# Optimization experiments

Hardware: AMD Instinct MI355X
Metric: run time of the kernel (lower is better)

Reference implementation:

```python
import jax, jax.numpy as jnp
import numpy as np

K = 16       # hidden size k
STATE = 8    # state_size

def _pre(x, W1, b1, W2, b2):
    # PreProcess: two Linear+ReLU layers
    return jax.nn.relu(jax.nn.relu(x @ W1 + b1) @ W2 + b2)

def _dblock(x, W1, b1, W2, b2, Wmu, bmu, Wls, bls):
    # DBlock (TD-VAE style): gated hidden then mu / logsigma heads
    t = jnp.tanh(x @ W1 + b1) * jax.nn.sigmoid(x @ W2 + b2)
    return t @ Wmu + bmu, t @ Wls + bls

def setup_inputs() -> dict:
    key = jax.random.key(0)
    ks = iter(jax.random.split(key, 40))
    L, B, IN, OBS = 1000, 1024, 8, 4
    def w(shape):
        return (jax.random.normal(next(ks), shape, jnp.float32) / np.sqrt(shape[0])).astype(jnp.float32)
    z = lambda n: jnp.zeros((n,), jnp.float32)
    return {
        "external_input_seq": jax.random.normal(next(ks), (L, B, IN), jnp.float32),
        "observations_seq":   jax.random.normal(next(ks), (L, B, OBS), jnp.float32),
        "eps":                jax.random.normal(next(ks), (L, B, STATE), jnp.float32),
        # process_u / process_x / process_z (PreProcess)
        "pu_W1": w((IN, K)),  "pu_b1": z(K), "pu_W2": w((K, K)), "pu_b2": z(K),
        "px_W1": w((OBS, K)), "px_b1": z(K), "px_W2": w((K, K)), "px_b2": z(K),
        "pz_W1": w((STATE, K)), "pz_b1": z(K), "pz_W2": w((K, K)), "pz_b2": z(K),
        # posterior_gauss: DBlock(3k, 3k, state_size)
        "post_W1": w((3*K, 3*K)), "post_b1": z(3*K),
        "post_W2": w((3*K, 3*K)), "post_b2": z(3*K),
        "post_Wmu": w((3*K, STATE)), "post_bmu": z(STATE),
        "post_Wls": w((3*K, STATE)), "post_bls": z(STATE),
        # rnn: tanh RNN cell, input 3k -> hidden k, 1 layer
        "rnn_Wih": w((3*K, K)), "rnn_bih": z(K),
        "rnn_Whh": w((K, K)),   "rnn_bhh": z(K),
    }

def reference(external_input_seq, observations_seq, eps,
              pu_W1, pu_b1, pu_W2, pu_b2,
              px_W1, px_b1, px_W2, px_b2,
              pz_W1, pz_b1, pz_W2, pz_b2,
              post_W1, post_b1, post_W2, post_b2,
              post_Wmu, post_bmu, post_Wls, post_bls,
              rnn_Wih, rnn_bih, rnn_Whh, rnn_bhh):
    # forward_posterior with memory_state=None
    L, B, _ = external_input_seq.shape
    u_e = _pre(external_input_seq, pu_W1, pu_b1, pu_W2, pu_b2)  # [L,B,K] (precomputed, as in torch)
    x_e = _pre(observations_seq, px_W1, px_b1, px_W2, px_b2)    # [L,B,K]
    h0 = jnp.zeros((B, K), external_input_seq.dtype)

    def step(h, inputs):
        xe_t, ue_t, eps_t = inputs  # [B,K],[B,K],[B,STATE]
        mu, ls = _dblock(jnp.concatenate([xe_t, ue_t, h], -1),
                         post_W1, post_b1, post_W2, post_b2,
                         post_Wmu, post_bmu, post_Wls, post_bls)
        # reparameterized sample from N(mu, diag(exp(ls))) -> std = exp(0.5*ls)
        z_t = mu + jnp.exp(0.5 * ls) * eps_t
        z_e = _pre(z_t, pz_W1, pz_b1, pz_W2, pz_b2)
        rnn_in = jnp.concatenate([xe_t, ue_t, z_e], -1)  # [B,3K]
        h_new = jnp.tanh(rnn_in @ rnn_Wih + rnn_bih + h @ rnn_Whh + rnn_bhh)
        return h_new, (mu, ls)

    h_final, (state_mu, state_logsigma) = jax.lax.scan(step, h0, (x_e, u_e, eps))
    # returns (state_mu, state_logsigma, memory_state hn); rnn_hidden == hn[None] for 1 layer
    return state_mu, state_logsigma, h_final
```

## Files before the change

### kernel.cpp

```cpp
#include <hip/hip_runtime.h>

#define L_STEPS 1000
#define BATCH   1024

__device__ __forceinline__ float frcp(float x)  { return __builtin_amdgcn_rcpf(x); }
__device__ __forceinline__ float fsig(float x)  { return frcp(1.0f + __expf(-x)); }
__device__ __forceinline__ float ftanh(float x) { return 1.0f - 2.0f * frcp(__expf(2.0f * x) + 1.0f); }

#define FMA4(vv, W, base, A) do { \
    A = fmaf((vv).x, W[(base)+0], A); \
    A = fmaf((vv).y, W[(base)+1], A); \
    A = fmaf((vv).z, W[(base)+2], A); \
    A = fmaf((vv).w, W[(base)+3], A); } while (0)

__global__ __launch_bounds__(64, 1) void vrnn_scan(
    const float* __restrict__ ext, const float* __restrict__ obs, const float* __restrict__ eps,
    const float* __restrict__ puW1, const float* __restrict__ pub1,
    const float* __restrict__ puW2, const float* __restrict__ pub2,
    const float* __restrict__ pxW1, const float* __restrict__ pxb1,
    const float* __restrict__ pxW2, const float* __restrict__ pxb2,
    const float* __restrict__ pzW1, const float* __restrict__ pzb1,
    const float* __restrict__ pzW2, const float* __restrict__ pzb2,
    const float* __restrict__ poW1, const float* __restrict__ pob1,
    const float* __restrict__ poW2, const float* __restrict__ pob2,
    const float* __restrict__ Wmu, const float* __restrict__ bmu,
    const float* __restrict__ Wls, const float* __restrict__ bls,
    const float* __restrict__ Wih, const float* __restrict__ bih,
    const float* __restrict__ Whh, const float* __restrict__ bhh,
    float* __restrict__ out)
{
    const int l   = threadIdx.x;
    const int r   = blockIdx.x;
    const int idx = l >> 2;
    const int p   = l & 3;

    __shared__ __align__(16) float rawbuf[16];
    __shared__ __align__(16) float epsbuf[8];
    __shared__ __align__(16) float h1buf[32];
    __shared__ __align__(16) float in64[64];
    __shared__ __align__(16) float s2buf[48];
    __shared__ __align__(16) float t48[48];
    __shared__ __align__(16) float zbuf[8];
    __shared__ __align__(16) float ze1buf[16];
    __shared__ float bheadb[16];
    __shared__ float brnnb[16];

    if (l < 16) {
        rawbuf[l]    = 0.0f;
        in64[48 + l] = 0.0f;
        bheadb[l]    = (l < 8) ? bmu[l] : bls[l - 8];
        brnnb[l]     = bih[l] + bhh[l];
    }

    float wA[48]; float biasA;
    {
        const float* baseA;
        if (l < 48) { baseA = poW1 + l;        biasA = pob1[l]; }
        else        { baseA = poW2 + (l - 48); biasA = pob2[l - 48]; }
        #pragma unroll
        for (int k = 0; k < 48; ++k) wA[k] = baseA[k * 48];
    }
    float wB[48]; float biasB;
    {
        const int c = 16 + (l & 31);
        const float* baseB = poW2 + c;
        biasB = pob2[c];
        #pragma unroll
        for (int k = 0; k < 48; ++k) wB[k] = baseB[k * 48];
    }
    float whead[12];
    {
        const float* baseH = (idx < 8) ? (Wmu + idx) : (Wls + (idx - 8));
        #pragma unroll
        for (int i = 0; i < 12; ++i) whead[i] = baseH[(12 * p + i) * 8];
    }
    float wrnn[16];
    {
        #pragma unroll
        for (int i = 0; i < 16; ++i) {
            const int c = 16 * p + i;
            const float a = Wih[min(c, 47) * 16 + idx];
            const float b = Whh[max(c - 48, 0) * 16 + idx];
            wrnn[i] = (c < 48) ? a : b;
        }
    }
    const int j16 = l & 15;
    float wpre1[8], wpre2[16], bpre1, bpre2;
    {
        const bool isx = (l < 16);
        #pragma unroll
        for (int k = 0; k < 8; ++k) {
            const float xv = pxW1[min(k, 3) * 16 + j16];
            const float uv = puW1[k * 16 + j16];
            float v = isx ? xv : uv;
            if (isx && k >= 4) v = 0.0f;
            wpre1[k] = v;
        }
        #pragma unroll
        for (int k = 0; k < 16; ++k) {
            const float xv = pxW2[k * 16 + j16];
            const float uv = puW2[k * 16 + j16];
            wpre2[k] = isx ? xv : uv;
        }
        bpre1 = isx ? pxb1[j16] : pub1[j16];
        bpre2 = isx ? pxb2[j16] : pub2[j16];
    }
    float wpz1[8], wpz2[16], bpz1, bpz2;
    {
        #pragma unroll
        for (int k = 0; k < 8; ++k)  wpz1[k] = pzW1[k * 16 + j16];
        #pragma unroll
        for (int k = 0; k < 16; ++k) wpz2[k] = pzW2[k * 16 + j16];
        bpz1 = pzb1[j16];
        bpz2 = pzb2[j16];
    }

    const float* pin; long pstride;
    if (l < 4)                  { pin = obs + (size_t)r * 4 + l;        pstride = 4 * BATCH; }
    else if (l >= 8 && l < 16)  { pin = ext + (size_t)r * 8 + (l - 8);  pstride = 8 * BATCH; }
    else if (l >= 16 && l < 24) { pin = eps + (size_t)r * 8 + (l - 16); pstride = 8 * BATCH; }
    else                        { pin = obs;                            pstride = 0; }

    float vin = *pin;
    pin += pstride;

    float* pout = out + ((idx < 8) ? ((size_t)r * 8 + idx)
                                   : ((size_t)L_STEPS * BATCH * 8 + (size_t)r * 8 + (idx - 8)));

    __syncthreads();

    float hn = 0.0f;

    for (int t = 0; t < L_STEPS; ++t) {
        if (l < 4 || (l >= 8 && l < 16)) rawbuf[l] = vin;
        if (l >= 16 && l < 24)           epsbuf[l - 16] = vin;
        vin = *pin;
        pin += (t < L_STEPS - 2) ? pstride : 0;

        {
            const float4* rb = (const float4*)(rawbuf + ((l & 16) ? 8 : 0));
            float4 v0 = rb[0], v1 = rb[1];
            float a1 = bpre1;
            FMA4(v0, wpre1, 0, a1);
            FMA4(v1, wpre1, 4, a1);
            a1 = fmaxf(a1, 0.0f);
            if (l < 32) h1buf[l] = a1;
            const float4* hb = (const float4*)(h1buf + ((l & 16) ? 16 : 0));
            float a2 = bpre2;
            #pragma unroll
            for (int q = 0; q < 4; ++q) { float4 v = hb[q]; FMA4(v, wpre2, 4 * q, a2); }
            a2 = fmaxf(a2, 0.0f);
            if (l < 32) in64[l] = a2;
        }

        float sA = biasA, sB = biasB;
        {
            const float4* c4 = (const float4*)in64;
            #pragma unroll
            for (int q = 0; q < 8; ++q) {
                float4 v = c4[q];
                FMA4(v, wA, 4 * q, sA);
                FMA4(v, wB, 4 * q, sB);
            }
            const float4* h4 = (const float4*)(in64 + 48);
            #pragma unroll
            for (int q = 0; q < 4; ++q) {
                float4 v = h4[q];
                FMA4(v, wA, 32 + 4 * q, sA);
                FMA4(v, wB, 32 + 4 * q, sB);
            }
        }
        if (l >= 48) s2buf[l - 48] = sA;
        if (l < 32)  s2buf[16 + l] = sB;
        if (l < 48)  t48[l] = ftanh(sA) * fsig(s2buf[l]);

        float acc = 0.0f;
        {
            const float4* tb = (const float4*)(t48 + 12 * p);
            float4 a0 = tb[0], a1v = tb[1], a2v = tb[2];
            FMA4(a0,  whead, 0, acc);
            FMA4(a1v, whead, 4, acc);
            FMA4(a2v, whead, 8, acc);
        }
        acc += __shfl_xor(acc, 1);
        acc += __shfl_xor(acc, 2);
        acc += bheadb[idx];
        if (p == 0) *pout = acc;
        pout += (size_t)8 * BATCH;

        {
            float lsv = __shfl(acc, l | 32);
            if (l < 32) {
                float z = fmaf(__expf(0.5f * lsv), epsbuf[idx], acc);
                if (p == 0) zbuf[idx] = z;
            }
        }

        {
            const float4* zb = (const float4*)zbuf;
            float4 z0 = zb[0], z1 = zb[1];
            float a1 = bpz1;
            FMA4(z0, wpz1, 0, a1);
            FMA4(z1, wpz1, 4, a1);
            a1 = fmaxf(a1, 0.0f);
            if (l < 16) ze1buf[l] = a1;
            const float4* zeb = (const float4*)ze1buf;
            float a2 = bpz2;
            #pragma unroll
            for (int q = 0; q < 4; ++q) { float4 v = zeb[q]; FMA4(v, wpz2, 4 * q, a2); }
            a2 = fmaxf(a2, 0.0f);
            if (l < 16) in64[32 + l] = a2;
        }

        {
            const float4* ib = (const float4*)(in64 + 16 * p);
            float a = 0.0f;
            #pragma unroll
            for (int q = 0; q < 4; ++q) { float4 v = ib[q]; FMA4(v, wrnn, 4 * q, a); }
            a += __shfl_xor(a, 1);
            a += __shfl_xor(a, 2);
            a += brnnb[idx];
            hn = ftanh(a);
            if (p == 0) in64[48 + idx] = hn;
        }
    }

    if (p == 0) out[(size_t)L_STEPS * BATCH * 8 * 2 + (size_t)r * 16 + idx] = hn;
}

extern "C" void kernel_launch(void* const* d_in, const int* in_sizes, int n_in,
                              void* d_out, int out_size, void* d_ws, size_t ws_size,
                              hipStream_t stream) {
    const float* ext  = (const float*)d_in[0];
    const float* obs  = (const float*)d_in[1];
    const float* eps  = (const float*)d_in[2];
    const float* puW1 = (const float*)d_in[3];  const float* pub1 = (const float*)d_in[4];
    const float* puW2 = (const float*)d_in[5];  const float* pub2 = (const float*)d_in[6];
    const float* pxW1 = (const float*)d_in[7];  const float* pxb1 = (const float*)d_in[8];
    const float* pxW2 = (const float*)d_in[9];  const float* pxb2 = (const float*)d_in[10];
    const float* pzW1 = (const float*)d_in[11]; const float* pzb1 = (const float*)d_in[12];
    const float* pzW2 = (const float*)d_in[13]; const float* pzb2 = (const float*)d_in[14];
    const float* poW1 = (const float*)d_in[15]; const float* pob1 = (const float*)d_in[16];
    const float* poW2 = (const float*)d_in[17]; const float* pob2 = (const float*)d_in[18];
    const float* Wmu  = (const float*)d_in[19]; const float* bmu  = (const float*)d_in[20];
    const float* Wls  = (const float*)d_in[21]; const float* bls  = (const float*)d_in[22];
    const float* Wih  = (const float*)d_in[23]; const float* bih  = (const float*)d_in[24];
    const float* Whh  = (const float*)d_in[25]; const float* bhh  = (const float*)d_in[26];
    float* out = (float*)d_out;

    vrnn_scan<<<dim3(BATCH), dim3(64), 0, stream>>>(
        ext, obs, eps,
        puW1, pub1, puW2, pub2,
        pxW1, pxb1, pxW2, pxb2,
        pzW1, pzb1, pzW2, pzb2,
        poW1, pob1, poW2, pob2,
        Wmu, bmu, Wls, bls,
        Wih, bih, Whh, bhh,
        out);
}
```

Measured before the change: 1.350 ms.

## Precompute time-parallel projections in a separate kernel before the recurrent scan

Adds a fully parallel pre-pass kernel that computes the x/u preprocessing plus their contributions to the posterior gates and the RNN input projection for every timestep, and stores them in a 128-float-per-row workspace. A new scan kernel then only does the h-dependent work each step: it reads the precomputed partial sums with one-step-ahead prefetch and uses DPP quad reductions and shuffles across a 4-lane split. This takes the non-recurrent matmuls off the serial critical path. In exchange it writes and reads roughly half a gigabyte of workspace, and it falls back to the old kernel when the workspace is too small.

```diff
diff --git a/kernel.cpp b/kernel.cpp
--- a/kernel.cpp
+++ b/kernel.cpp
@@ -2,16 +2,242 @@
 
 #define L_STEPS 1000
 #define BATCH   1024
+#define REC     128
 
 __device__ __forceinline__ float frcp(float x)  { return __builtin_amdgcn_rcpf(x); }
 __device__ __forceinline__ float fsig(float x)  { return frcp(1.0f + __expf(-x)); }
 __device__ __forceinline__ float ftanh(float x) { return 1.0f - 2.0f * frcp(__expf(2.0f * x) + 1.0f); }
+
+__device__ __forceinline__ float qxor1(float x) {
+    return __int_as_float(__builtin_amdgcn_update_dpp(0, __float_as_int(x), 0xB1, 0xF, 0xF, true));
+}
+__device__ __forceinline__ float qxor2(float x) {
+    return __int_as_float(__builtin_amdgcn_update_dpp(0, __float_as_int(x), 0x4E, 0xF, 0xF, true));
+}
 
 #define FMA4(vv, W, base, A) do { \
     A = fmaf((vv).x, W[(base)+0], A); \
     A = fmaf((vv).y, W[(base)+1], A); \
     A = fmaf((vv).z, W[(base)+2], A); \
     A = fmaf((vv).w, W[(base)+3], A); } while (0)
+
+__global__ __launch_bounds__(128) void vrnn_pre(
+    const float* __restrict__ ext, const float* __restrict__ obs,
+    const float* __restrict__ puW1, const float* __restrict__ pub1,
+    const float* __restrict__ puW2, const float* __restrict__ pub2,
+    const float* __restrict__ pxW1, const float* __restrict__ pxb1,
+    const float* __restrict__ pxW2, const float* __restrict__ pxb2,
+    const float* __restrict__ poW1, const float* __restrict__ pob1,
+    const float* __restrict__ poW2, const float* __restrict__ pob2,
+    const float* __restrict__ Wih, const float* __restrict__ bih,
+    const float* __restrict__ bhh,
+    float* __restrict__ ws)
+{
+    const int j  = threadIdx.x;
+    const int rc = blockIdx.x * 128;
+    const int t  = blockIdx.y;
+
+    __shared__ float wsm[768];
+    __shared__ float xu[128][36];
+
+    for (int i = j; i < 64;  i += 128) wsm[0   + i] = pxW1[i];
+    for (int i = j; i < 256; i += 128) wsm[64  + i] = pxW2[i];
+    for (int i = j; i < 128; i += 128) wsm[320 + i] = puW1[i];
+    for (int i = j; i < 256; i += 128) wsm[448 + i] = puW2[i];
+    if (j < 16) {
+        wsm[704 + j] = pxb1[j]; wsm[720 + j] = pxb2[j];
+        wsm[736 + j] = pub1[j]; wsm[752 + j] = pub2[j];
+    }
+    __syncthreads();
+
+    {
+        const size_t row = (size_t)t * BATCH + rc + j;
+        const float* o = obs + row * 4;
+        const float* e = ext + row * 8;
+        float ob[4], ex[8];
+        #pragma unroll
+        for (int k = 0; k < 4; ++k) ob[k] = o[k];
+        #pragma unroll
+        for (int k = 0; k < 8; ++k) ex[k] = e[k];
+
+        float t1[16];
+        #pragma unroll
+        for (int c = 0; c < 16; ++c) {
+            float a = wsm[704 + c];
+            #pragma unroll
+            for (int k = 0; k < 4; ++k) a = fmaf(ob[k], wsm[0 + k * 16 + c], a);
+            t1[c] = fmaxf(a, 0.0f);
+        }
+        #pragma unroll
+        for (int c = 0; c < 16; ++c) {
+            float a = wsm[720 + c];
+            #pragma unroll
+            for (int k = 0; k < 16; ++k) a = fmaf(t1[k], wsm[64 + k * 16 + c], a);
+            xu[j][c] = fmaxf(a, 0.0f);
+        }
+        #pragma unroll
+        for (int c = 0; c < 16; ++c) {
+            float a = wsm[736 + c];
+            #pragma unroll
+            for (int k = 0; k < 8; ++k) a = fmaf(ex[k], wsm[320 + k * 16 + c], a);
+            t1[c] = fmaxf(a, 0.0f);
+        }
+        #pragma unroll
+        for (int c = 0; c < 16; ++c) {
+            float a = wsm[752 + c];
+            #pragma unroll
+            for (int k = 0; k < 16; ++k) a = fmaf(t1[k], wsm[448 + k * 16 + c], a);
+            xu[j][16 + c] = fmaxf(a, 0.0f);
+        }
+    }
+
+    float wc[32]; float bias = 0.0f;
+    if (j < 96) {
+        const int c = j >> 1;
+        const float* W = (j & 1) ? poW2 : poW1;
+        bias = (j & 1) ? pob2[c] : pob1[c];
+        #pragma unroll
+        for (int k = 0; k < 32; ++k) wc[k] = W[k * 48 + c];
+    } else if (j < 112) {
+        const int c = j - 96;
+        bias = bih[c] + bhh[c];
+        #pragma unroll
+        for (int k = 0; k < 32; ++k) wc[k] = Wih[k * 16 + c];
+    } else {
+        #pragma unroll
+        for (int k = 0; k < 32; ++k) wc[k] = 0.0f;
+    }
+    __syncthreads();
+
+    float* rb = ws + ((size_t)t * BATCH + rc) * REC + j;
+    for (int r = 0; r < 128; ++r) {
+        const float4* x4 = (const float4*)&xu[r][0];
+        float a = bias;
+        #pragma unroll
+        for (int q = 0; q < 8; ++q) { float4 v = x4[q]; FMA4(v, wc, 4 * q, a); }
+        rb[(size_t)r * REC] = a;
+    }
+}
+
+__global__ __launch_bounds__(64, 1) void vrnn_scan2(
+    const float* __restrict__ ws, const float* __restrict__ eps,
+    const float* __restrict__ poW1, const float* __restrict__ poW2,
+    const float* __restrict__ Wmu, const float* __restrict__ bmu,
+    const float* __restrict__ Wls, const float* __restrict__ bls,
+    const float* __restrict__ pzW1, const float* __restrict__ pzb1,
+    const float* __restrict__ pzW2, const float* __restrict__ pzb2,
+    const float* __restrict__ Wih, const float* __restrict__ Whh,
+    float* __restrict__ out)
+{
+    const int l   = threadIdx.x;
+    const int r   = blockIdx.x;
+    const int idx = l >> 2;
+    const int p   = l & 3;
+
+    const int cl = (l < 48) ? l : 47;
+    float wAh[16], wBh[16];
+    #pragma unroll
+    for (int k = 0; k < 16; ++k) {
+        wAh[k] = poW1[(32 + k) * 48 + cl];
+        wBh[k] = poW2[(32 + k) * 48 + cl];
+    }
+    const int hm = idx & 7;
+    const float* WH = (idx < 8) ? Wmu : Wls;
+    float whead[12];
+    #pragma unroll
+    for (int i = 0; i < 12; ++i) whead[i] = WH[(12 * p + i) * 8 + hm];
+    const float bhead = (idx < 8) ? bmu[hm] : bls[hm];
+
+    float wr[8];
+    #pragma unroll
+    for (int i = 0; i < 8; ++i)
+        wr[i] = (p < 2) ? Wih[(32 + 8 * (p & 1) + i) * 16 + idx]
+                        : Whh[(8 * (p & 1) + i) * 16 + idx];
+
+    const float wz1a = pzW1[(2 * p) * 16 + idx];
+    const float wz1b = pzW1[(2 * p + 1) * 16 + idx];
+    const float bz1  = pzb1[idx];
+    float wz2[4];
+    #pragma unroll
+    for (int i = 0; i < 4; ++i) wz2[i] = pzW2[(4 * p + i) * 16 + idx];
+    const float bz2 = pzb2[idx];
+
+    const float* recp = ws + (size_t)r * REC + ((l < 48) ? 2 * l : 48 + l);
+    const size_t rstride = (size_t)BATCH * REC;
+    const float* epsp = eps + (size_t)r * 8 + (l & 7);
+
+    float2 f2 = make_float2(0.0f, 0.0f); float d1 = 0.0f;
+    if (l < 48) f2 = *(const float2*)recp; else d1 = *recp;
+    float ev = *epsp;
+    recp += rstride; epsp += (size_t)8 * BATCH;
+
+    float* pout = out + ((idx < 8) ? ((size_t)r * 8 + idx)
+                                   : ((size_t)L_STEPS * BATCH * 8 + (size_t)r * 8 + (idx - 8)));
+
+    float h[16];
+    #pragma unroll
+    for (int k = 0; k < 16; ++k) h[k] = 0.0f;
+    float hn = 0.0f;
+
+    for (int t = 0; t < L_STEPS; ++t) {
+        const float s1p = f2.x, s2p = f2.y;
+        const float ihpv = d1, epsv = ev;
+
+        float2 nf2 = make_float2(0.0f, 0.0f); float nd1 = 0.0f;
+        if (l < 48) nf2 = *(const float2*)recp; else nd1 = *recp;
+        float nev = *epsp;
+        recp += (t < L_STEPS - 2) ? rstride : 0;
+        epsp += (t < L_STEPS - 2) ? (size_t)8 * BATCH : 0;
+
+        const float ihg = __shfl(ihpv, 48 + idx);
+        const float eg  = __shfl(epsv, idx & 7);
+
+        #pragma unroll
+        for (int k = 0; k < 16; ++k) h[k] = __shfl(hn, 4 * k);
+        float sA = s1p, sB = s2p;
+        #pragma unroll
+        for (int k = 0; k < 16; ++k) {
+            sA = fmaf(h[k], wAh[k], sA);
+            sB = fmaf(h[k], wBh[k], sB);
+        }
+        const float tt = ftanh(sA) * fsig(sB);
+
+        float acc = 0.0f;
+        #pragma unroll
+        for (int i = 0; i < 12; ++i) acc = fmaf(__shfl(tt, 12 * p + i), whead[i], acc);
+        acc += qxor1(acc); acc += qxor2(acc);
+        acc += bhead;
+        if (p == 0) *pout = acc;
+        pout += (size_t)8 * BATCH;
+
+        const float other = __shfl(acc, l ^ 32);
+        const float zv = fmaf(__expf(0.5f * other), eg, acc);
+
+        float a1 = fmaf(__shfl(zv, 8 * p), wz1a, __shfl(zv, 8 * p + 4) * wz1b);
+        a1 += qxor1(a1); a1 += qxor2(a1);
+        a1 = fmaxf(a1 + bz1, 0.0f);
+
+        float ze = 0.0f;
+        #pragma unroll
+        for (int i = 0; i < 4; ++i) ze = fmaf(__shfl(a1, 16 * p + 4 * i), wz2[i], ze);
+        ze += qxor1(ze); ze += qxor2(ze);
+        ze = fmaxf(ze + bz2, 0.0f);
+
+        float pre = 0.0f;
+        #pragma unroll
+        for (int i = 0; i < 8; ++i) {
+            const float g = __shfl(ze, 4 * (8 * (p & 1) + i));
+            const float v = (p < 2) ? g : h[8 * (p & 1) + i];
+            pre = fmaf(v, wr[i], pre);
+        }
+        pre += qxor1(pre); pre += qxor2(pre);
+        hn = ftanh(pre + ihg);
+
+        f2 = nf2; d1 = nd1; ev = nev;
+    }
+
+    if (p == 0) out[(size_t)L_STEPS * BATCH * 8 * 2 + (size_t)r * 16 + idx] = hn;
+}
 
 __global__ __launch_bounds__(64, 1) void vrnn_scan(
     const float* __restrict__ ext, const float* __restrict__ obs, const float* __restrict__ eps,
@@ -248,13 +474,24 @@
     const float* Whh  = (const float*)d_in[25]; const float* bhh  = (const float*)d_in[26];
     float* out = (float*)d_out;
 
-    vrnn_scan<<<dim3(BATCH), dim3(64), 0, stream>>>(
-        ext, obs, eps,
-        puW1, pub1, puW2, pub2,
-        pxW1, pxb1, pxW2, pxb2,
-        pzW1, pzb1, pzW2, pzb2,
-        poW1, pob1, poW2, pob2,
-        Wmu, bmu, Wls, bls,
-        Wih, bih, Whh, bhh,
-        out);
-}
+    const size_t need = (size_t)L_STEPS * BATCH * REC * sizeof(float);
+    if (ws_size >= need) {
+        float* ws = (float*)d_ws;
+        vrnn_pre<<<dim3(BATCH / 128, L_STEPS), dim3(128), 0, stream>>>(
+            ext, obs, puW1, pub1, puW2, pub2, pxW1, pxb1, pxW2, pxb2,
+            poW1, pob1, poW2, pob2, Wih, bih, bhh, ws);
+        vrnn_scan2<<<dim3(BATCH), dim3(64), 0, stream>>>(
+            ws, eps, poW1, poW2, Wmu, bmu, Wls, bls,
+            pzW1, pzb1, pzW2, pzb2, Wih, Whh, out);
+    } else {
+        vrnn_scan<<<dim3(BATCH), dim3(64), 0, stream>>>(
+            ext, obs, eps,
+            puW1, pub1, puW2, pub2,
+            pxW1, pxb1, pxW2, pxb2,
+            pzW1, pzb1, pzW2, pzb2,
+            poW1, pob1, poW2, pob2,
+            Wmu, bmu, Wls, bls,
+            Wih, bih, Whh, bhh,
+            out);
+    }
+}
```

Measured after the change: 1.348 ms. Within noise of the previous version (-0.1%).
